# Optimization experiments

Hardware: AMD Instinct MI355X
Metric: run time of the kernel (lower is better)

The kernel has to match this reference:

```python
import jax, jax.numpy as jnp
import numpy as np

WS = 7          # window size
SHIFT = 3       # shift size (SW-MSA)
NH = 4          # num heads
EPS = 1e-5      # LayerNorm eps (torch default)


def _rel_pos_index(ws):
    coords = np.stack(np.meshgrid(np.arange(ws), np.arange(ws), indexing='ij'))  # (2, ws, ws)
    cf = coords.reshape(2, -1)                      # (2, ws*ws)
    rel = cf[:, :, None] - cf[:, None, :]           # (2, N, N)
    rel = rel.transpose(1, 2, 0)
    rel[:, :, 0] += ws - 1
    rel[:, :, 1] += ws - 1
    rel[:, :, 0] *= 2 * ws - 1
    return jnp.asarray(rel.sum(-1))                 # (N, N) int

REL_IDX = _rel_pos_index(WS)


def _shift_mask(Hp, Wp, ws, shift):
    """Standard Swin attention mask for shifted windows: (nW, N, N) float32."""
    img = np.zeros((1, Hp, Wp, 1), dtype=np.float32)
    cnt = 0
    sl = (slice(0, -ws), slice(-ws, -shift), slice(-shift, None))
    for h in sl:
        for w in sl:
            img[:, h, w, :] = cnt
            cnt += 1
    win = img.reshape(1, Hp // ws, ws, Wp // ws, ws, 1).transpose(0, 1, 3, 2, 4, 5)
    win = win.reshape(-1, ws * ws)                  # (nW, N)
    m = win[:, None, :] - win[:, :, None]
    return jnp.asarray(np.where(m != 0, -100.0, 0.0).astype(np.float32))


def _ln(x, g, b):
    mu = jnp.mean(x, -1, keepdims=True)
    var = jnp.mean(jnp.square(x - mu), -1, keepdims=True)
    return (x - mu) * jax.lax.rsqrt(var + EPS) * g + b


def _win_partition(x, ws):
    B, H, W, C = x.shape
    x = x.reshape(B, H // ws, ws, W // ws, ws, C).transpose(0, 1, 3, 2, 4, 5)
    return x.reshape(-1, ws * ws, C)


def _win_reverse(w, ws, B, H, W):
    C = w.shape[-1]
    x = w.reshape(B, H // ws, W // ws, ws, ws, C).transpose(0, 1, 3, 2, 4, 5)
    return x.reshape(B, H, W, C)


def setup_inputs() -> dict:
    key = jax.random.key(0)
    ks = jax.random.split(key, 12)
    B, H, W, C = 16, 112, 112, 128
    hid = 4 * C
    std = 0.02
    inp = {
        'x': jax.random.normal(ks[0], (B, H * W, C), jnp.float32),
        'H': H, 'W': W,
        'attn_mask': _shift_mask(H, W, WS, SHIFT),
        'ln1_g': jnp.ones((C,), jnp.float32),
        'ln1_b': jnp.zeros((C,), jnp.float32),
        'qkv_w': jax.random.normal(ks[1], (3 * C, C), jnp.float32) * std,
        'qkv_b': jnp.zeros((3 * C,), jnp.float32),
        'rel_bias_table': jax.random.normal(ks[2], ((2 * WS - 1) ** 2, NH), jnp.float32) * std,
        'proj_w': jax.random.normal(ks[3], (C, C), jnp.float32) * std,
        'proj_b': jnp.zeros((C,), jnp.float32),
        'ln2_g': jnp.ones((C,), jnp.float32),
        'ln2_b': jnp.zeros((C,), jnp.float32),
        'fc1_w': jax.random.normal(ks[4], (hid, C), jnp.float32) * std,
        'fc1_b': jnp.zeros((hid,), jnp.float32),
        'fc2_w': jax.random.normal(ks[5], (C, hid), jnp.float32) * std,
        'fc2_b': jnp.zeros((C,), jnp.float32),
    }
    return inp


def reference(x, H, W, attn_mask, ln1_g, ln1_b, qkv_w, qkv_b, rel_bias_table,
              proj_w, proj_b, ln2_g, ln2_b, fc1_w, fc1_b, fc2_w, fc2_b):
    B, L, C = x.shape
    N = WS * WS
    hd = C // NH
    scale = hd ** -0.5

    shortcut = x
    h = _ln(x, ln1_g, ln1_b).reshape(B, H, W, C)
    # H, W chosen divisible by WS -> no padding branch needed
    h = jnp.roll(h, shift=(-SHIFT, -SHIFT), axis=(1, 2))
    xw = _win_partition(h, WS)                      # (B_, N, C), B_ = B*nW
    B_ = xw.shape[0]
    nW = attn_mask.shape[0]

    qkv = xw @ qkv_w.T + qkv_b                      # (B_, N, 3C)
    qkv = qkv.reshape(B_, N, 3, NH, hd).transpose(2, 0, 3, 1, 4)
    q, k, v = qkv[0], qkv[1], qkv[2]                # (B_, NH, N, hd)

    attn = jnp.einsum('bhnd,bhmd->bhnm', q, k) * scale
    bias = rel_bias_table[REL_IDX]                  # (N, N, NH)
    attn = attn + bias.transpose(2, 0, 1)[None]     # (B_, NH, N, N)
    attn = attn.reshape(B_ // nW, nW, NH, N, N) + attn_mask[None, :, None]
    attn = jax.nn.softmax(attn.reshape(B_, NH, N, N), axis=-1)

    o = jnp.einsum('bhnm,bhmd->bhnd', attn, v)      # (B_, NH, N, hd)
    o = o.transpose(0, 2, 1, 3).reshape(B_, N, C)
    o = o @ proj_w.T + proj_b

    h = _win_reverse(o, WS, B, H, W)
    h = jnp.roll(h, shift=(SHIFT, SHIFT), axis=(1, 2))
    x1 = shortcut + h.reshape(B, L, C)

    f = _ln(x1, ln2_g, ln2_b)
    f = jax.nn.gelu(f @ fc1_w.T + fc1_b, approximate=False)
    f = f @ fc2_w.T + fc2_b
    return x1 + f
```

## Files before the change

### kernel.cpp

```cpp
#include <hip/hip_runtime.h>
#include <hip/hip_bf16.h>
#include <math.h>

#define B_IMG 16
#define HH 112
#define WW_ 112
#define CC 128
#define LL (HH*WW_)
#define BWIN 4096
#define NTOK 49
#define NROWS (BWIN*NTOK)
#define HD 32
#define SCALE 0.1767766952966369f
#define SHIFT_ 3

typedef short bf16x8 __attribute__((ext_vector_type(8)));
typedef float f32x4 __attribute__((ext_vector_type(4)));
typedef unsigned short ushort_t;

__device__ __forceinline__ float wave_sum(float v) {
#pragma unroll
  for (int off = 32; off >= 1; off >>= 1) v += __shfl_xor(v, off, 64);
  return v;
}

__device__ __forceinline__ float gelu_f(float x) {
  float x3 = x * x * x;
  float y = 0.7978845608028654f * fmaf(0.044715f, x3, x);
  float e = __expf(2.f * y);
  float th = 1.f - 2.f / (e + 1.f);
  return 0.5f * x * (1.f + th);
}

__global__ __launch_bounds__(256) void castw_kernel(const float* __restrict__ w,
                                                    __hip_bfloat16* __restrict__ o, int n) {
  int i = blockIdx.x * 256 + threadIdx.x;
  if (i < n) o[i] = __float2bfloat16(w[i]);
}

__global__ __launch_bounds__(256) void prep_bias(const float* __restrict__ table,
                                                 float* __restrict__ biasPad) {
  int idx = blockIdx.x * 256 + threadIdx.x;
  int h = idx >> 12, q = (idx >> 6) & 63, k = idx & 63;
  float v = 0.f;
  if (q < NTOK && k < NTOK) {
    int yi = q / 7, xi = q % 7, yj = k / 7, xj = k % 7;
    v = table[((yi - yj + 6) * 13 + (xi - xj + 6)) * 4 + h];
  }
  biasPad[idx] = v;
}

__global__ __launch_bounds__(256) void prep_mask(const float* __restrict__ mask,
                                                 float* __restrict__ maskPad) {
  int idx = blockIdx.x * 256 + threadIdx.x;
  int pat = idx >> 12, q = (idx >> 6) & 63, k = idx & 63;
  float v = -1e30f;
  if (q < NTOK && k < NTOK) v = mask[pat * (NTOK * NTOK) + q * NTOK + k];
  maskPad[idx] = v;
}

template<bool GATHER>
__global__ __launch_bounds__(256) void ln_kernel(
    const float* __restrict__ X, const float* __restrict__ g,
    const float* __restrict__ b, __hip_bfloat16* __restrict__ Y)
{
  int wid  = threadIdx.x >> 6;
  int lane = threadIdx.x & 63;
  int r = blockIdx.x * 4 + wid;
  size_t src;
  if (GATHER) {
    int win = r / NTOK, n = r % NTOK;
    int bi = win >> 8, wi = win & 255;
    int wh = wi >> 4, wwi = wi & 15;
    int ii = n / 7, jj = n % 7;
    int hp = wh * 7 + ii, wp = wwi * 7 + jj;
    int sh = (hp + SHIFT_) % HH, sw = (wp + SHIFT_) % WW_;
    src = ((size_t)bi * LL + (size_t)sh * WW_ + sw) * CC;
  } else {
    src = (size_t)r * CC;
  }
  float v0 = X[src + lane];
  float v1 = X[src + 64 + lane];
  float mean = wave_sum(v0 + v1) * (1.f / CC);
  float d0 = v0 - mean, d1 = v1 - mean;
  float var = wave_sum(d0 * d0 + d1 * d1) * (1.f / CC);
  float rstd = rsqrtf(var + 1e-5f);
  size_t dst = (size_t)r * CC;
  Y[dst + lane]      = __float2bfloat16(d0 * rstd * g[lane]      + b[lane]);
  Y[dst + 64 + lane] = __float2bfloat16(d1 * rstd * g[lane + 64] + b[lane + 64]);
}

enum { EPI_BIAS = 0, EPI_GELU = 1, EPI_RES = 2, EPI_PROJ = 3 };
#define LDSW 136

#define STAGE_A(KB)                                                              \
  _Pragma("unroll")                                                              \
  for (int p = 0; p < 8; ++p) {                                                  \
    int lin = p * 256 + t;                                                       \
    int row = lin >> 4;                                                          \
    int col = (lin & 15) * 8;                                                    \
    *(uint4*)&As[row * LDSW + col] =                                             \
        *(const uint4*)(A + (size_t)(m0 + row) * K + (KB) + col);                \
  }

#define STAGE_B(NOFF, KB)                                                        \
  _Pragma("unroll")                                                              \
  for (int p = 0; p < 8; ++p) {                                                  \
    int lin = p * 256 + t;                                                       \
    int row = lin >> 4;                                                          \
    int col = (lin & 15) * 8;                                                    \
    *(uint4*)&Bs[row * LDSW + col] =                                             \
        *(const uint4*)(W + (size_t)((NOFF) + row) * K + (KB) + col);            \
  }

#define MFMA_BLOCK                                                               \
  _Pragma("unroll")                                                              \
  for (int ks = 0; ks < 4; ++ks) {                                               \
    int k0 = ks * 32 + quad * 8;                                                 \
    bf16x8 af[4], bf[4];                                                         \
    _Pragma("unroll")                                                            \
    for (int i = 0; i < 4; ++i)                                                  \
      af[i] = *(const bf16x8*)&As[(wr + i * 16 + l16) * LDSW + k0];              \
    _Pragma("unroll")                                                            \
    for (int j = 0; j < 4; ++j)                                                  \
      bf[j] = *(const bf16x8*)&Bs[(wc + j * 16 + l16) * LDSW + k0];              \
    _Pragma("unroll")                                                            \
    for (int i = 0; i < 4; ++i)                                                  \
      _Pragma("unroll")                                                          \
      for (int j = 0; j < 4; ++j)                                                \
        acc[i][j] = __builtin_amdgcn_mfma_f32_16x16x32_bf16(af[i], bf[j],        \
                                                            acc[i][j], 0, 0, 0); \
  }

template<int EPI, int NB, bool LNF>
__global__ __launch_bounds__(256, 2) void gemm_bf16(
    const ushort_t* __restrict__ A, const ushort_t* __restrict__ W,
    const float* __restrict__ bias, const float* __restrict__ aux,
    void* __restrict__ outp, const float* __restrict__ g2,
    const float* __restrict__ b2, __hip_bfloat16* __restrict__ ln_out,
    int N, int K)
{
  __shared__ ushort_t As[128 * LDSW];
  __shared__ ushort_t Bs[128 * LDSW];
  int t = threadIdx.x;
  int lane = t & 63;
  int quad = lane >> 4;
  int l16  = lane & 15;
  int wr = (t >> 7) * 64;
  int wc = ((t >> 6) & 1) * 64;
  int m0 = blockIdx.x * 128;

  f32x4 acc[4][4];

  for (int nb = 0; nb < NB; ++nb) {
    int n_off = (NB == 1) ? blockIdx.y * 128 : nb * 128;
#pragma unroll
    for (int i = 0; i < 4; ++i)
#pragma unroll
      for (int j = 0; j < 4; ++j) acc[i][j] = (f32x4){0.f, 0.f, 0.f, 0.f};

    if (NB == 1) {
      for (int kb = 0; kb < K; kb += 128) {
        if (kb) __syncthreads();
        STAGE_A(kb);
        STAGE_B(n_off, kb);
        __syncthreads();
        MFMA_BLOCK;
      }
    } else {
      if (nb == 0) { STAGE_A(0); STAGE_B(0, 0); }
      __syncthreads();
      MFMA_BLOCK;
      __syncthreads();
      if (nb + 1 < NB) { STAGE_B((nb + 1) * 128, 0); }
    }

    if (EPI == EPI_PROJ) {
      float s[4][4], ss[4][4];
      unsigned rowB[4][4];
#pragma unroll
      for (int i = 0; i < 4; ++i) {
#pragma unroll
        for (int r = 0; r < 4; ++r) {
          s[i][r] = 0.f; ss[i][r] = 0.f;
          int m = m0 + wr + i * 16 + quad * 4 + r;
          int win = m / NTOK, nn = m % NTOK;
          int bi = win >> 8, wi = win & 255;
          int wh = wi >> 4, wwi = wi & 15;
          int ii = nn / 7, jj = nn % 7;
          int hp = wh * 7 + ii, wp = wwi * 7 + jj;
          int oh = (hp + SHIFT_) % HH, ow = (wp + SHIFT_) % WW_;
          unsigned base = ((unsigned)bi * LL + (unsigned)oh * WW_ + ow) * CC;
          rowB[i][r] = base;
#pragma unroll
          for (int j = 0; j < 4; ++j) {
            int n = wc + j * 16 + l16;
            float x1 = aux[base + n] + acc[i][j][r] + bias[n];
            ((float*)outp)[base + n] = x1;
            if (LNF) {
              acc[i][j][r] = x1;
              s[i][r] += x1;
              ss[i][r] = fmaf(x1, x1, ss[i][r]);
            }
          }
        }
      }
      if (LNF) {
#pragma unroll
        for (int i = 0; i < 4; ++i)
#pragma unroll
          for (int r = 0; r < 4; ++r) {
#pragma unroll
            for (int off = 8; off >= 1; off >>= 1) {
              s[i][r]  += __shfl_xor(s[i][r],  off, 64);
              ss[i][r] += __shfl_xor(ss[i][r], off, 64);
            }
          }
        float* red = (float*)As;
        __syncthreads();
        if (l16 == 0) {
#pragma unroll
          for (int i = 0; i < 4; ++i)
#pragma unroll
            for (int r = 0; r < 4; ++r) {
              int ml = wr + i * 16 + quad * 4 + r;
              red[((wc >> 6) * 128 + ml) * 2 + 0] = s[i][r];
              red[((wc >> 6) * 128 + ml) * 2 + 1] = ss[i][r];
            }
        }
        __syncthreads();
#pragma unroll
        for (int i = 0; i < 4; ++i)
#pragma unroll
          for (int r = 0; r < 4; ++r) {
            int ml = wr + i * 16 + quad * 4 + r;
            float st  = red[ml * 2 + 0] + red[(128 + ml) * 2 + 0];
            float sst = red[ml * 2 + 1] + red[(128 + ml) * 2 + 1];
            float mean = st * (1.f / 128.f);
            float var  = sst * (1.f / 128.f) - mean * mean;
            s[i][r]  = mean;
            ss[i][r] = rsqrtf(var + 1e-5f);
          }
#pragma unroll
        for (int i = 0; i < 4; ++i)
#pragma unroll
          for (int r = 0; r < 4; ++r) {
            unsigned base = rowB[i][r];
#pragma unroll
            for (int j = 0; j < 4; ++j) {
              int n = wc + j * 16 + l16;
              float ln = (acc[i][j][r] - s[i][r]) * ss[i][r] * g2[n] + b2[n];
              ln_out[(size_t)base + n] = __float2bfloat16(ln);
            }
          }
      }
    } else {
#pragma unroll
      for (int i = 0; i < 4; ++i) {
#pragma unroll
        for (int j = 0; j < 4; ++j) {
          int n = n_off + wc + j * 16 + l16;
          float bn = bias[n];
#pragma unroll
          for (int reg = 0; reg < 4; ++reg) {
            int m = m0 + wr + i * 16 + quad * 4 + reg;
            float v = acc[i][j][reg] + bn;
            if (EPI == EPI_BIAS) {
              ((__hip_bfloat16*)outp)[(size_t)m * N + n] = __float2bfloat16(v);
            } else if (EPI == EPI_GELU) {
              v = gelu_f(v);
              ((__hip_bfloat16*)outp)[(size_t)m * N + n] = __float2bfloat16(v);
            } else {
              ((float*)outp)[(size_t)m * N + n] = v + aux[(size_t)m * N + n];
            }
          }
        }
      }
    }
  }
}

__global__ __launch_bounds__(256, 2) void mlp_fused(
    const ushort_t* __restrict__ A,
    const ushort_t* __restrict__ W1,
    const float* __restrict__ b1,
    const ushort_t* __restrict__ W2,
    const float* __restrict__ b2,
    float* __restrict__ out)
{
  __shared__ ushort_t As[64 * LDSW];
  __shared__ ushort_t Bs[128 * LDSW];
  __shared__ ushort_t Hs[64 * LDSW];
  int t = threadIdx.x;
  int lane = t & 63;
  int quad = lane >> 4;
  int l16  = lane & 15;
  int wr = (t >> 7) * 32;
  int wc = ((t >> 6) & 1) * 64;
  int m0 = blockIdx.x * 64;

#pragma unroll
  for (int p = 0; p < 4; ++p) {
    int lin = p * 256 + t;
    int row = lin >> 4, col = (lin & 15) * 8;
    *(uint4*)&As[row * LDSW + col] = *(const uint4*)(A + (size_t)(m0 + row) * 128 + col);
  }

  f32x4 acc2[2][4];
#pragma unroll
  for (int i = 0; i < 2; ++i)
#pragma unroll
    for (int j = 0; j < 4; ++j) acc2[i][j] = (f32x4){0.f, 0.f, 0.f, 0.f};

  for (int nb = 0; nb < 4; ++nb) {
    __syncthreads();
#pragma unroll
    for (int p = 0; p < 8; ++p) {
      int lin = p * 256 + t;
      int row = lin >> 4, col = (lin & 15) * 8;
      *(uint4*)&Bs[row * LDSW + col] =
          *(const uint4*)(W1 + (size_t)(nb * 128 + row) * 128 + col);
    }
    __syncthreads();
    f32x4 acc1[2][4];
#pragma unroll
    for (int i = 0; i < 2; ++i)
#pragma unroll
      for (int j = 0; j < 4; ++j) acc1[i][j] = (f32x4){0.f, 0.f, 0.f, 0.f};
#pragma unroll
    for (int ks = 0; ks < 4; ++ks) {
      int k0 = ks * 32 + quad * 8;
      bf16x8 af[2], bf[4];
#pragma unroll
      for (int i = 0; i < 2; ++i)
        af[i] = *(const bf16x8*)&As[(wr + i * 16 + l16) * LDSW + k0];
#pragma unroll
      for (int j = 0; j < 4; ++j)
        bf[j] = *(const bf16x8*)&Bs[(wc + j * 16 + l16) * LDSW + k0];
#pragma unroll
      for (int i = 0; i < 2; ++i)
#pragma unroll
        for (int j = 0; j < 4; ++j)
          acc1[i][j] = __builtin_amdgcn_mfma_f32_16x16x32_bf16(af[i], bf[j], acc1[i][j], 0, 0, 0);
    }
    __syncthreads();
#pragma unroll
    for (int i = 0; i < 2; ++i)
#pragma unroll
      for (int j = 0; j < 4; ++j) {
        int hc = wc + j * 16 + l16;
        float bn = b1[nb * 128 + hc];
#pragma unroll
        for (int r = 0; r < 4; ++r) {
          int hr = wr + i * 16 + quad * 4 + r;
          float v = gelu_f(acc1[i][j][r] + bn);
          *(__hip_bfloat16*)&Hs[hr * LDSW + hc] = __float2bfloat16(v);
        }
      }
#pragma unroll
    for (int p = 0; p < 8; ++p) {
      int lin = p * 256 + t;
      int row = lin >> 4, col = (lin & 15) * 8;
      *(uint4*)&Bs[row * LDSW + col] =
          *(const uint4*)(W2 + (size_t)row * 512 + nb * 128 + col);
    }
    __syncthreads();
#pragma unroll
    for (int ks = 0; ks < 4; ++ks) {
      int k0 = ks * 32 + quad * 8;
      bf16x8 hf[2], wf[4];
#pragma unroll
      for (int i = 0; i < 2; ++i)
        hf[i] = *(const bf16x8*)&Hs[(wr + i * 16 + l16) * LDSW + k0];
#pragma unroll
      for (int j = 0; j < 4; ++j)
        wf[j] = *(const bf16x8*)&Bs[(wc + j * 16 + l16) * LDSW + k0];
#pragma unroll
      for (int i = 0; i < 2; ++i)
#pragma unroll
        for (int j = 0; j < 4; ++j)
          acc2[i][j] = __builtin_amdgcn_mfma_f32_16x16x32_bf16(hf[i], wf[j], acc2[i][j], 0, 0, 0);
    }
  }

#pragma unroll
  for (int i = 0; i < 2; ++i)
#pragma unroll
    for (int j = 0; j < 4; ++j) {
      int n = wc + j * 16 + l16;
      float bn = b2[n];
#pragma unroll
      for (int r = 0; r < 4; ++r) {
        int m = m0 + wr + i * 16 + quad * 4 + r;
        out[(size_t)m * 128 + n] += acc2[i][j][r] + bn;
      }
    }
}

#define WLDS 6656

__global__ __launch_bounds__(256) void attn_mfma(
    const ushort_t* __restrict__ qkv, const float* __restrict__ maskPad,
    const float* __restrict__ biasPad, __hip_bfloat16* __restrict__ O, int win_off)
{
  __shared__ ushort_t lds[4 * WLDS];
  const int win_l = blockIdx.x;
  const int win_g = win_off + win_l;
  const int h    = threadIdx.x >> 6;
  const int lane = threadIdx.x & 63;
  const int quad = lane >> 4;
  const int l16  = lane & 15;
  ushort_t* wb = lds + h * WLDS;
  ushort_t* Vt = wb + 4608;

  {
    const int tok = lane;
    uint4 z = make_uint4(0u, 0u, 0u, 0u);
    uint4 k0 = z, k1 = z, k2 = z, k3 = z;
    union { uint4 v4[4]; ushort_t u[32]; } vv;
    vv.v4[0] = z; vv.v4[1] = z; vv.v4[2] = z; vv.v4[3] = z;
    if (tok < NTOK) {
      const ushort_t* src = qkv + ((size_t)win_l * NTOK + tok) * 384 + h * HD;
      k0 = *(const uint4*)(src + 128); k1 = *(const uint4*)(src + 136);
      k2 = *(const uint4*)(src + 144); k3 = *(const uint4*)(src + 152);
      vv.v4[0] = *(const uint4*)(src + 256); vv.v4[1] = *(const uint4*)(src + 264);
      vv.v4[2] = *(const uint4*)(src + 272); vv.v4[3] = *(const uint4*)(src + 280);
    }
    *(uint4*)&wb[tok * 40 +  0] = k0;
    *(uint4*)&wb[tok * 40 +  8] = k1;
    *(uint4*)&wb[tok * 40 + 16] = k2;
    *(uint4*)&wb[tok * 40 + 24] = k3;
#pragma unroll
    for (int d = 0; d < 32; ++d) Vt[d * 64 + tok] = vv.u[d];
  }

  bf16x8 qf[4];
  {
    const ushort_t* qb = qkv + (size_t)win_l * NTOK * 384 + h * HD + quad * 8;
#pragma unroll
    for (int i = 0; i < 4; ++i)
      qf[i] = *(const bf16x8*)(qb + (size_t)(i * 16 + l16) * 384);
  }

  f32x4 S[4][4];
#pragma unroll
  for (int i = 0; i < 4; ++i)
#pragma unroll
    for (int j = 0; j < 4; ++j) S[i][j] = (f32x4){0.f, 0.f, 0.f, 0.f};
  bf16x8 kf[4];
#pragma unroll
  for (int j = 0; j < 4; ++j)
    kf[j] = *(const bf16x8*)&wb[(j * 16 + l16) * 40 + quad * 8];
#pragma unroll
  for (int i = 0; i < 4; ++i)
#pragma unroll
    for (int j = 0; j < 4; ++j)
      S[i][j] = __builtin_amdgcn_mfma_f32_16x16x32_bf16(qf[i], kf[j], S[i][j], 0, 0, 0);

  const float* mrow = maskPad + (size_t)(win_g & 255) * 4096;
  const float* brow = biasPad + (size_t)h * 4096;
#pragma unroll
  for (int i = 0; i < 4; ++i)
#pragma unroll
    for (int j = 0; j < 4; ++j)
#pragma unroll
      for (int r = 0; r < 4; ++r) {
        int q = i * 16 + quad * 4 + r;
        int k = j * 16 + l16;
        S[i][j][r] = fmaf(S[i][j][r], SCALE, brow[q * 64 + k] + mrow[q * 64 + k]);
      }

  float inv[4][4];
#pragma unroll
  for (int i = 0; i < 4; ++i)
#pragma unroll
    for (int r = 0; r < 4; ++r) {
      float mx = fmaxf(fmaxf(S[i][0][r], S[i][1][r]), fmaxf(S[i][2][r], S[i][3][r]));
      mx = fmaxf(mx, __shfl_xor(mx, 1, 64));
      mx = fmaxf(mx, __shfl_xor(mx, 2, 64));
      mx = fmaxf(mx, __shfl_xor(mx, 4, 64));
      mx = fmaxf(mx, __shfl_xor(mx, 8, 64));
      float sum = 0.f;
#pragma unroll
      for (int j = 0; j < 4; ++j) {
        float e = __expf(S[i][j][r] - mx);
        S[i][j][r] = e;
        sum += e;
      }
      sum += __shfl_xor(sum, 1, 64);
      sum += __shfl_xor(sum, 2, 64);
      sum += __shfl_xor(sum, 4, 64);
      sum += __shfl_xor(sum, 8, 64);
      inv[i][r] = 1.f / sum;
    }

#pragma unroll
  for (int i = 0; i < 4; ++i)
#pragma unroll
    for (int j = 0; j < 4; ++j)
#pragma unroll
      for (int r = 0; r < 4; ++r) {
        int q = i * 16 + quad * 4 + r;
        int k = j * 16 + l16;
        *(__hip_bfloat16*)&wb[q * 72 + k] = __float2bfloat16(S[i][j][r]);
      }

  f32x4 Oacc[4][2];
#pragma unroll
  for (int i = 0; i < 4; ++i) {
    Oacc[i][0] = (f32x4){0.f, 0.f, 0.f, 0.f};
    Oacc[i][1] = (f32x4){0.f, 0.f, 0.f, 0.f};
  }
  bf16x8 vf[2][2];
#pragma unroll
  for (int ks = 0; ks < 2; ++ks)
#pragma unroll
    for (int jp = 0; jp < 2; ++jp)
      vf[ks][jp] = *(const bf16x8*)&Vt[(jp * 16 + l16) * 64 + ks * 32 + quad * 8];
#pragma unroll
  for (int i = 0; i < 4; ++i)
#pragma unroll
    for (int ks = 0; ks < 2; ++ks) {
      bf16x8 pf = *(const bf16x8*)&wb[(i * 16 + l16) * 72 + ks * 32 + quad * 8];
#pragma unroll
      for (int jp = 0; jp < 2; ++jp)
        Oacc[i][jp] = __builtin_amdgcn_mfma_f32_16x16x32_bf16(pf, vf[ks][jp], Oacc[i][jp], 0, 0, 0);
    }

  __hip_bfloat16* ob = O + ((size_t)win_g * NTOK) * CC + h * HD;
#pragma unroll
  for (int i = 0; i < 4; ++i)
#pragma unroll
    for (int r = 0; r < 4; ++r) {
      int q = i * 16 + quad * 4 + r;
      if (q < NTOK) {
        float sc = inv[i][r];
#pragma unroll
        for (int jp = 0; jp < 2; ++jp)
          ob[(size_t)q * CC + jp * 16 + l16] = __float2bfloat16(Oacc[i][jp][r] * sc);
      }
    }
}

extern "C" void kernel_launch(void* const* d_in, const int* in_sizes, int n_in,
                              void* d_out, int out_size, void* d_ws, size_t ws_size,
                              hipStream_t stream) {
  const float* x        = (const float*)d_in[0];
  const float* attnmask = (const float*)d_in[3];
  const float* ln1_g    = (const float*)d_in[4];
  const float* ln1_b    = (const float*)d_in[5];
  const float* qkv_w    = (const float*)d_in[6];
  const float* qkv_b    = (const float*)d_in[7];
  const float* table    = (const float*)d_in[8];
  const float* proj_w   = (const float*)d_in[9];
  const float* proj_b   = (const float*)d_in[10];
  const float* ln2_g    = (const float*)d_in[11];
  const float* ln2_b    = (const float*)d_in[12];
  const float* fc1_w    = (const float*)d_in[13];
  const float* fc1_b    = (const float*)d_in[14];
  const float* fc2_w    = (const float*)d_in[15];
  const float* fc2_b    = (const float*)d_in[16];
  float* out = (float*)d_out;

  const size_t bufA_elems = (size_t)NROWS * CC;
  const size_t bufB_full  = (size_t)NROWS * 384;
  const size_t bufB_chunk = (size_t)(NROWS / 2) * 384;
  const size_t bufC_elems = (size_t)NROWS * CC;
  const size_t w_elems    = 384*128 + 128*128 + 512*128 + 128*512;
  const size_t tbl_floats = 4 * 4096 + 256 * 4096;
  const size_t need_full  =
      (bufA_elems + bufB_full + bufC_elems + w_elems) * 2 + tbl_floats * 4;
  const bool full = ws_size >= need_full;

  __hip_bfloat16* bufA = (__hip_bfloat16*)d_ws;
  __hip_bfloat16* bufB = bufA + bufA_elems;
  __hip_bfloat16* bufC;
  __hip_bfloat16* wq;
  if (full) {
    bufC = bufB + bufB_full;
    wq   = bufC + bufC_elems;
  } else {
    bufC = nullptr;
    wq   = bufB + bufB_chunk;
  }
  __hip_bfloat16* wp   = wq + 384 * 128;
  __hip_bfloat16* w1   = wp + 128 * 128;
  __hip_bfloat16* w2   = w1 + 512 * 128;
  float* biasPad = (float*)(w2 + 128 * 512);
  float* maskPad = biasPad + 4 * 4096;

  castw_kernel<<<(384 * 128 + 255) / 256, 256, 0, stream>>>(qkv_w, wq, 384 * 128);
  castw_kernel<<<(128 * 128 + 255) / 256, 256, 0, stream>>>(proj_w, wp, 128 * 128);
  castw_kernel<<<(512 * 128 + 255) / 256, 256, 0, stream>>>(fc1_w, w1, 512 * 128);
  castw_kernel<<<(128 * 512 + 255) / 256, 256, 0, stream>>>(fc2_w, w2, 128 * 512);
  prep_bias<<<64, 256, 0, stream>>>(table, biasPad);
  prep_mask<<<4096, 256, 0, stream>>>(attnmask, maskPad);

  ln_kernel<true><<<NROWS / 4, 256, 0, stream>>>(x, ln1_g, ln1_b, bufA);

  if (full) {
    dim3 g(NROWS / 128, 1);
    gemm_bf16<EPI_BIAS, 3, false><<<g, 256, 0, stream>>>(
        (const ushort_t*)bufA, (const ushort_t*)wq, qkv_b, nullptr, bufB,
        nullptr, nullptr, nullptr, 384, 128);
    attn_mfma<<<BWIN, 256, 0, stream>>>((const ushort_t*)bufB, maskPad, biasPad,
                                        bufA, 0);
    gemm_bf16<EPI_PROJ, 1, true><<<g, 256, 0, stream>>>(
        (const ushort_t*)bufA, (const ushort_t*)wp, proj_b, x, out,
        ln2_g, ln2_b, bufC, 128, 128);
    mlp_fused<<<NROWS / 64, 256, 0, stream>>>(
        (const ushort_t*)bufC, (const ushort_t*)w1, fc1_b,
        (const ushort_t*)w2, fc2_b, out);
  } else {
    for (int c = 0; c < 2; ++c) {
      const int MC = NROWS / 2;
      const ushort_t* Ain = (const ushort_t*)(bufA + (size_t)c * MC * CC);
      dim3 g(MC / 128, 1);
      gemm_bf16<EPI_BIAS, 3, false><<<g, 256, 0, stream>>>(
          Ain, (const ushort_t*)wq, qkv_b, nullptr, bufB,
          nullptr, nullptr, nullptr, 384, 128);
      attn_mfma<<<2048, 256, 0, stream>>>((const ushort_t*)bufB, maskPad, biasPad,
                                          bufA, c * 2048);
    }
    {
      dim3 g(NROWS / 128, 1);
      gemm_bf16<EPI_PROJ, 1, false><<<g, 256, 0, stream>>>(
          (const ushort_t*)bufA, (const ushort_t*)wp, proj_b, x, out,
          nullptr, nullptr, nullptr, 128, 128);
    }
    ln_kernel<false><<<NROWS / 4, 256, 0, stream>>>(out, ln2_g, ln2_b, bufA);
    for (int c = 0; c < 4; ++c) {
      const int MC = NROWS / 4;
      const ushort_t* Ain = (const ushort_t*)(bufA + (size_t)c * MC * CC);
      float* Oc = out + (size_t)c * MC * CC;
      dim3 g1(MC / 128, 1);
      gemm_bf16<EPI_GELU, 4, false><<<g1, 256, 0, stream>>>(
          Ain, (const ushort_t*)w1, fc1_b, nullptr, bufB,
          nullptr, nullptr, nullptr, 512, 128);
      dim3 g2(MC / 128, 1);
      gemm_bf16<EPI_RES, 1, false><<<g2, 256, 0, stream>>>(
          (const ushort_t*)bufB, (const ushort_t*)w2, fc2_b, Oc, Oc,
          nullptr, nullptr, nullptr, 128, 512);
    }
  }
}
```

Before: 612.6 us.

## Read MLP weights directly from global memory and swizzle LDS tiles in mlp_fused

The fused MLP kernel no longer stages W1/W2 tiles through shared memory. Each wave loads its bf16x8 weight fragments straight from global memory, which relies on L2/L1 caching of the small weight matrices, and several block-wide barriers are dropped. The A and H tiles switch from padded LDS rows to an XOR-swizzled layout to avoid bank conflicts. With the smaller LDS footprint, launch bounds rise to 3 blocks per CU, which adds register pressure and makes the kernel more sensitive to global load latency on the weights.

```diff
diff --git a/kernel.cpp b/kernel.cpp
--- a/kernel.cpp
+++ b/kernel.cpp
@@ -280,7 +280,11 @@
   }
 }
 
-__global__ __launch_bounds__(256, 2) void mlp_fused(
+__device__ __forceinline__ const bf16x8* swz_r(const ushort_t* base, int row, int colbyte) {
+  return (const bf16x8*)((const char*)base + row * 256 + (colbyte ^ ((row & 7) << 4)));
+}
+
+__global__ __launch_bounds__(256, 3) void mlp_fused(
     const ushort_t* __restrict__ A,
     const ushort_t* __restrict__ W1,
     const float* __restrict__ b1,
@@ -288,9 +292,8 @@
     const float* __restrict__ b2,
     float* __restrict__ out)
 {
-  __shared__ ushort_t As[64 * LDSW];
-  __shared__ ushort_t Bs[128 * LDSW];
-  __shared__ ushort_t Hs[64 * LDSW];
+  __shared__ ushort_t As[64 * 128];
+  __shared__ ushort_t Hs[64 * 128];
   int t = threadIdx.x;
   int lane = t & 63;
   int quad = lane >> 4;
@@ -302,9 +305,12 @@
 #pragma unroll
   for (int p = 0; p < 4; ++p) {
     int lin = p * 256 + t;
-    int row = lin >> 4, col = (lin & 15) * 8;
-    *(uint4*)&As[row * LDSW + col] = *(const uint4*)(A + (size_t)(m0 + row) * 128 + col);
-  }
+    int row = lin >> 4;
+    int cb  = (lin & 15) * 16;
+    *(uint4*)((char*)As + row * 256 + (cb ^ ((row & 7) << 4))) =
+        *(const uint4*)(A + (size_t)(m0 + row) * 128 + (lin & 15) * 8);
+  }
+  __syncthreads();
 
   f32x4 acc2[2][4];
 #pragma unroll
@@ -312,16 +318,8 @@
 #pragma unroll
     for (int j = 0; j < 4; ++j) acc2[i][j] = (f32x4){0.f, 0.f, 0.f, 0.f};
 
+#pragma unroll
   for (int nb = 0; nb < 4; ++nb) {
-    __syncthreads();
-#pragma unroll
-    for (int p = 0; p < 8; ++p) {
-      int lin = p * 256 + t;
-      int row = lin >> 4, col = (lin & 15) * 8;
-      *(uint4*)&Bs[row * LDSW + col] =
-          *(const uint4*)(W1 + (size_t)(nb * 128 + row) * 128 + col);
-    }
-    __syncthreads();
     f32x4 acc1[2][4];
 #pragma unroll
     for (int i = 0; i < 2; ++i)
@@ -332,11 +330,11 @@
       int k0 = ks * 32 + quad * 8;
       bf16x8 af[2], bf[4];
 #pragma unroll
+      for (int j = 0; j < 4; ++j)
+        bf[j] = *(const bf16x8*)(W1 + (size_t)(nb * 128 + wc + j * 16 + l16) * 128 + k0);
+#pragma unroll
       for (int i = 0; i < 2; ++i)
-        af[i] = *(const bf16x8*)&As[(wr + i * 16 + l16) * LDSW + k0];
-#pragma unroll
-      for (int j = 0; j < 4; ++j)
-        bf[j] = *(const bf16x8*)&Bs[(wc + j * 16 + l16) * LDSW + k0];
+        af[i] = *swz_r(As, wr + i * 16 + l16, k0 * 2);
 #pragma unroll
       for (int i = 0; i < 2; ++i)
 #pragma unroll
@@ -354,27 +352,21 @@
         for (int r = 0; r < 4; ++r) {
           int hr = wr + i * 16 + quad * 4 + r;
           float v = gelu_f(acc1[i][j][r] + bn);
-          *(__hip_bfloat16*)&Hs[hr * LDSW + hc] = __float2bfloat16(v);
+          *(__hip_bfloat16*)((char*)Hs + hr * 256 + ((hc * 2) ^ ((hr & 7) << 4))) =
+              __float2bfloat16(v);
         }
       }
-#pragma unroll
-    for (int p = 0; p < 8; ++p) {
-      int lin = p * 256 + t;
-      int row = lin >> 4, col = (lin & 15) * 8;
-      *(uint4*)&Bs[row * LDSW + col] =
-          *(const uint4*)(W2 + (size_t)row * 512 + nb * 128 + col);
-    }
     __syncthreads();
 #pragma unroll
     for (int ks = 0; ks < 4; ++ks) {
       int k0 = ks * 32 + quad * 8;
       bf16x8 hf[2], wf[4];
 #pragma unroll
+      for (int j = 0; j < 4; ++j)
+        wf[j] = *(const bf16x8*)(W2 + (size_t)(wc + j * 16 + l16) * 512 + nb * 128 + k0);
+#pragma unroll
       for (int i = 0; i < 2; ++i)
-        hf[i] = *(const bf16x8*)&Hs[(wr + i * 16 + l16) * LDSW + k0];
-#pragma unroll
-      for (int j = 0; j < 4; ++j)
-        wf[j] = *(const bf16x8*)&Bs[(wc + j * 16 + l16) * LDSW + k0];
+        hf[i] = *swz_r(Hs, wr + i * 16 + l16, k0 * 2);
 #pragma unroll
       for (int i = 0; i < 2; ++i)
 #pragma unroll
```

Result: slower. 678.4 us (+10.7%).
